# Optimization experiments

Hardware: AMD Instinct MI355X
Metric: run time of the kernel (lower is better)

Reference implementation:

```python
import jax, jax.numpy as jnp
import numpy as np

N_NODES = 80000
N_EDGES = 1280000
IN_C, HID_C, OUT_C = 3, 64, 3
BN_EPS = 1e-5
LEAKY_SLOPE = 0.01  # torch LeakyReLU default
SELF_LOOP_W = 2.0   # GCNConv(improved=True) fill value


def gcn_conv(x, src, dst, n, W, b):
    # PyG GCNConv: x = x @ W, then degree-normalized aggregation with
    # self-loops of weight 2 (improved=True), then + bias.
    h = x @ W  # [N, out]
    deg = jnp.zeros((n,), x.dtype).at[dst].add(1.0) + SELF_LOOP_W  # in-degree + self loop weight
    dinv = jax.lax.rsqrt(deg)
    norm = dinv[src] * dinv[dst]  # per-edge norm (edge_weight = 1)
    agg = jax.ops.segment_sum(h[src] * norm[:, None], dst, num_segments=n)
    self_term = (SELF_LOOP_W * dinv * dinv)[:, None] * h  # self-loop contribution
    return agg + self_term + b


def batch_norm(x, gamma, beta):
    # training-mode BN over the node dimension, biased variance, eps=1e-5
    mean = jnp.mean(x, axis=0)
    var = jnp.mean((x - mean) ** 2, axis=0)
    return (x - mean) * jax.lax.rsqrt(var + BN_EPS) * gamma + beta


def maxpool1d(x, k, p):
    # torch MaxPool1d on a 2D [N, C] tensor pools along C (same-size: stride 1)
    return jax.lax.reduce_window(x, -jnp.inf, jax.lax.max,
                                 (1, k), (1, 1), ((0, 0), (p, p)))


def leaky_relu(x):
    return jnp.where(x >= 0, x, LEAKY_SLOPE * x)


def stage(x, src, dst, n, W, b, gamma, beta, lw, lb, pool_k, pool_p):
    h = gcn_conv(x, src, dst, n, W, b)
    h = batch_norm(h, gamma, beta)
    h = leaky_relu(maxpool1d(h, pool_k, pool_p))
    h = leaky_relu(h @ lw.T + lb)
    return h  # Dropout: eval-mode identity


def setup_inputs() -> dict:
    key = jax.random.key(0)
    ks = jax.random.split(key, 24)
    x = jax.random.normal(ks[0], (N_NODES, IN_C), dtype=jnp.float32)
    edge_index = jax.random.randint(ks[1], (2, N_EDGES), 0, N_NODES, dtype=jnp.int64)

    def lin_init(k, fan_in, shape):
        bound = 1.0 / np.sqrt(fan_in)
        return jax.random.uniform(k, shape, jnp.float32, -bound, bound)

    dims = [(IN_C, HID_C), (HID_C, HID_C), (HID_C, OUT_C)]
    params = {}
    i = 2
    for s, (cin, cout) in enumerate(dims):
        params[f"w{s}"] = lin_init(ks[i], cin, (cin, cout)); i += 1
        params[f"b{s}"] = jnp.zeros((cout,), jnp.float32)
        params[f"g{s}"] = jnp.ones((cout,), jnp.float32)
        params[f"bb{s}"] = jnp.zeros((cout,), jnp.float32)
        params[f"lw{s}"] = lin_init(ks[i], cout, (cout, cout)); i += 1
        params[f"lb{s}"] = lin_init(ks[i], cout, (cout,)); i += 1
    return {"x": x, "edge_index": edge_index, **params}


def reference(x, edge_index, w0, b0, g0, bb0, lw0, lb0,
              w1, b1, g1, bb1, lw1, lb1,
              w2, b2, g2, bb2, lw2, lb2):
    src, dst = edge_index[0], edge_index[1]
    n = x.shape[0]
    h = stage(x, src, dst, n, w0, b0, g0, bb0, lw0, lb0, 3, 1)
    h = stage(h, src, dst, n, w1, b1, g1, bb1, lw1, lb1, 5, 2)
    h = stage(h, src, dst, n, w2, b2, g2, bb2, lw2, lb2, 3, 1)
    return h
```

## Files before the change

kernel.cpp:

```cpp
#include <hip/hip_runtime.h>
#include <hip/hip_bf16.h>
#include <math.h>

#define N_NODES 80000
#define N_EDGES 1280000
#define CHUNK 128
#define N_CHUNKS (N_EDGES / CHUNK)
#define NCB 64
#define CB_DIV 1250
#define CB_CAP 21000
#define NFB 1250
#define FB_CAP 1280
#define EPB 1280
#define ATS 20

typedef __hip_bfloat16 bf16;

__device__ __forceinline__ float leaky(float x) { return x >= 0.f ? x : 0.01f * x; }

union U4 { uint4 v; bf16 h[8]; };


__global__ void k_init(float* bnsums, float* bnrep, int* ctails, int* ftails,
                       const float* __restrict__ lw0, const float* __restrict__ w1,
                       const float* __restrict__ lw1, uint4* __restrict__ pkw) {
    int i = blockIdx.x * 256 + threadIdx.x;
    if (i < 384) bnsums[i] = 0.f;
    if (i < 2048) bnrep[i] = 0.f;
    if (i < NCB) ctails[i] = 0;
    if (i < NFB) ftails[i] = 0;
    if (i >= 1536) return;
    int set = i >> 9, r = i & 511;
    int k = r >> 3, cg = r & 7;
    U4 u;
    if (set == 0) {
#pragma unroll
        for (int j = 0; j < 8; ++j) u.h[j] = __float2bfloat16(lw0[(cg * 8 + j) * 64 + k]);
    } else if (set == 1) {
#pragma unroll
        for (int j = 0; j < 8; ++j) u.h[j] = __float2bfloat16(w1[k * 64 + cg * 8 + j]);
    } else {
#pragma unroll
        for (int j = 0; j < 8; ++j) u.h[j] = __float2bfloat16(lw1[(cg * 8 + j) * 64 + k]);
    }
    pkw[i] = u.v;
}

__global__ void __launch_bounds__(256)
k_part(const int* __restrict__ ei, unsigned int* __restrict__ cpairs,
       int* __restrict__ ctails) {
    __shared__ int cnt[NCB], off[NCB];
    int t = threadIdx.x;
    if (t < NCB) cnt[t] = 0;
    __syncthreads();
    int base = blockIdx.x * EPB;
    unsigned int loc[5];
    int blk[5];
#pragma unroll
    for (int u = 0; u < 5; ++u) {
        int e = base + u * 256 + t;
        int s = ei[e], d = ei[N_EDGES + e];
        int b = d / CB_DIV;
        blk[u] = b;
        loc[u] = (unsigned int)s | ((unsigned int)(d - b * CB_DIV) << 17);
        atomicAdd(&cnt[b], 1);
    }
    __syncthreads();
    if (t < NCB) off[t] = atomicAdd(&ctails[t], cnt[t]);
    __syncthreads();
#pragma unroll
    for (int u = 0; u < 5; ++u) {
        int b = blk[u];
        int pos = atomicAdd(&off[b], 1);
        cpairs[(size_t)b * CB_CAP + pos] = loc[u];
    }
}

__global__ void __launch_bounds__(256)
k_refine(const unsigned int* __restrict__ cpairs, const int* __restrict__ ctails,
         int* __restrict__ ftails, unsigned int* __restrict__ fpairs) {
    __shared__ unsigned int s_ed[2048];
    __shared__ unsigned int s_comp[2048];
    __shared__ int cnt2[32], off2[32], lcl[32], lpos[32];
    int b = blockIdx.x & 63;
    int j = blockIdx.x >> 6;
    int t = threadIdx.x;
    int cnt = ctails[b];
    int s0 = j * 2048;
    if (s0 >= cnt) return;
    int n = min(2048, cnt - s0);
    int fb0 = (b * CB_DIV) >> 6;
    int nbins = (((b + 1) * CB_DIV - 1) >> 6) - fb0 + 1;
    int dbase = b * CB_DIV;
    const unsigned int* lst = cpairs + (size_t)b * CB_CAP + s0;
    for (int i = t; i < n; i += 256) s_ed[i] = lst[i];
    if (t < 32) cnt2[t] = 0;
    __syncthreads();
    for (int i = t; i < n; i += 256) {
        int d = dbase + (int)(s_ed[i] >> 17);
        atomicAdd(&cnt2[(d >> 6) - fb0], 1);
    }
    __syncthreads();
    if (t == 0) {
        int s = 0;
        for (int q = 0; q < nbins; ++q) { lcl[q] = s; s += cnt2[q]; }
    }
    if (t < nbins && cnt2[t] > 0) off2[t] = atomicAdd(&ftails[fb0 + t], cnt2[t]);
    __syncthreads();
    if (t < nbins) lpos[t] = lcl[t];
    __syncthreads();
    for (int i = t; i < n; i += 256) {
        unsigned int r = s_ed[i];
        int d = dbase + (int)(r >> 17);
        int fbl = (d >> 6) - fb0;
        int p = atomicAdd(&lpos[fbl], 1);
        s_comp[p] = (r & 0x1FFFFu) | ((unsigned int)(d & 63) << 20);
    }
    __syncthreads();
    int wv = t >> 6, ln = t & 63;
    for (int q = wv; q < nbins; q += 4) {
        int c = cnt2[q];
        if (c == 0) continue;
        unsigned int* dst = fpairs + (size_t)(fb0 + q) * FB_CAP + off2[q];
        const unsigned int* src = s_comp + lcl[q];
        for (int i = ln; i < c; i += 64) dst[i] = src[i];
    }
}

__global__ void k_scanF(const int* __restrict__ ftails, int* __restrict__ fbase) {
    __shared__ int csum[256];
    int t = threadIdx.x;
    int loc[5];
    int sum = 0;
#pragma unroll
    for (int u = 0; u < 5; ++u) {
        int idx = t * 5 + u;
        int v = (idx < NFB) ? ftails[idx] : 0;
        loc[u] = sum;
        sum += v;
    }
    csum[t] = sum;
    __syncthreads();
    for (int off = 1; off < 256; off <<= 1) {
        int x = (t >= off) ? csum[t - off] : 0;
        __syncthreads();
        csum[t] += x;
        __syncthreads();
    }
    int base = (t > 0) ? csum[t - 1] : 0;
#pragma unroll
    for (int u = 0; u < 5; ++u) {
        int idx = t * 5 + u;
        if (idx < NFB) fbase[idx] = base + loc[u];
    }
}

__global__ void __launch_bounds__(256)
k_sortfine(const unsigned int* __restrict__ fpairs, const int* __restrict__ ftails,
           const int* __restrict__ fbase, int2* __restrict__ ed2,
           float* __restrict__ dinv, int* __restrict__ cursor) {
    __shared__ unsigned int stage[FB_CAP];
    __shared__ int hist[64], cur[64];
    int fb = blockIdx.x;
    int t = threadIdx.x;
    int cnt = ftails[fb];
    int base = fbase[fb];
    int node0 = fb * 64;
    const unsigned int* lst = fpairs + (size_t)fb * FB_CAP;
    if (t < 64) hist[t] = 0;
    __syncthreads();
    for (int i = t; i < cnt; i += 256)
        atomicAdd(&hist[lst[i] >> 20], 1);
    __syncthreads();
    if (t == 0) {
        int s = 0;
        for (int j = 0; j < 64; ++j) { cur[j] = s; s += hist[j]; }
    }
    __syncthreads();
    if (t < 64) {
        cursor[node0 + t] = base + cur[t];
        dinv[node0 + t] = rsqrtf((float)hist[t] + 2.0f);
    }
    __syncthreads();
    for (int i = t; i < cnt; i += 256) {
        unsigned int r = lst[i];
        int p = atomicAdd(&cur[r >> 20], 1);
        stage[p] = r;
    }
    __syncthreads();
    for (int i = t; i < cnt; i += 256) {
        unsigned int r = stage[i];
        ed2[base + i] = make_int2((int)(r & 0xFFFFFu), node0 + (int)(r >> 20));
    }
}

__global__ void k_h0(const float* __restrict__ x, const float* __restrict__ W0,
                     const float* __restrict__ dinv, bf16* __restrict__ hs) {
    int tid = blockIdx.x * blockDim.x + threadIdx.x;
    if (tid < N_NODES * 64) {
        int v = tid >> 6, c = tid & 63;
        float x0 = x[v * 3], x1 = x[v * 3 + 1], x2 = x[v * 3 + 2];
        float h = x0 * W0[c] + x1 * W0[64 + c] + x2 * W0[128 + c];
        hs[tid] = __float2bfloat16(dinv[v] * h);
    }
}


__global__ void __launch_bounds__(256)
k_aggf(const bf16* __restrict__ hs, const int2* __restrict__ ed2,
       const float* __restrict__ dinv, const float* __restrict__ bias,
       float* __restrict__ y, float* __restrict__ bnrep) {
    int lane = threadIdx.x & 63;
    int wid = (blockIdx.x * blockDim.x + threadIdx.x) >> 6;
    float bc = bias[lane];
    float bs = 0.f, bss = 0.f;
    if (wid < N_CHUNKS) {
        int e = wid * CHUNK;
        int dp = (e == 0) ? -1 : ed2[e - 1].y;
        int cur = dp;
        float acc = 0.f;
        float selfv = 0.f, dvc = 0.f;
        int2 c[8];
#pragma unroll
        for (int u = 0; u < 8; ++u) c[u] = ed2[e + u];
        for (int b = 0; b < CHUNK / 8; ++b) {
            float pv[8];
#pragma unroll
            for (int u = 0; u < 8; ++u)
                pv[u] = __bfloat162float(hs[(size_t)c[u].x * 64 + lane]);
            int2 cn[8];
            if (b < CHUNK / 8 - 1) {
#pragma unroll
                for (int u = 0; u < 8; ++u) cn[u] = ed2[e + 8 + u];
            }
#pragma unroll
            for (int u = 0; u < 8; ++u) {
                int du = __builtin_amdgcn_readfirstlane(c[u].y);
                if (du != cur) {
                    if (cur != dp) {
                        float yf = fmaf(dvc, acc + 2.f * selfv, bc);
                        y[(size_t)cur * 64 + lane] = yf;
                        bs += yf; bss += yf * yf;
                    }
                    for (int g = cur + 1; g < du; ++g) {
                        float yf = fmaf(dinv[g],
                                        2.f * __bfloat162float(hs[(size_t)g * 64 + lane]), bc);
                        y[(size_t)g * 64 + lane] = yf;
                        bs += yf; bss += yf * yf;
                    }
                    cur = du;
                    acc = 0.f;
                    selfv = __bfloat162float(hs[(size_t)du * 64 + lane]);
                    dvc = dinv[du];
                }
                acc += pv[u];
            }
            e += 8;
            if (b < CHUNK / 8 - 1) {
#pragma unroll
                for (int u = 0; u < 8; ++u) c[u] = cn[u];
            }
        }
        while (e < N_EDGES) {
            int2 ct[8];
            float pt[8];
#pragma unroll
            for (int u = 0; u < 8; ++u) ct[u] = ed2[min(e + u, N_EDGES - 1)];
#pragma unroll
            for (int u = 0; u < 8; ++u)
                pt[u] = __bfloat162float(hs[(size_t)ct[u].x * 64 + lane]);
            bool contin = true;
#pragma unroll
            for (int u = 0; u < 8; ++u) {
                if (contin && e + u < N_EDGES &&
                    __builtin_amdgcn_readfirstlane(ct[u].y) == cur)
                    acc += pt[u];
                else
                    contin = false;
            }
            e += 8;
            if (!contin) break;
        }
        if (cur != dp) {
            float yf = fmaf(dvc, acc + 2.f * selfv, bc);
            y[(size_t)cur * 64 + lane] = yf;
            bs += yf; bss += yf * yf;
        }
        if (wid == N_CHUNKS - 1) {
            for (int g = cur + 1; g < N_NODES; ++g) {
                float yf = fmaf(dinv[g],
                                2.f * __bfloat162float(hs[(size_t)g * 64 + lane]), bc);
                y[(size_t)g * 64 + lane] = yf;
                bs += yf; bss += yf * yf;
            }
        }
    }
    __shared__ float s1[256], s2[256];
    s1[threadIdx.x] = bs;
    s2[threadIdx.x] = bss;
    __syncthreads();
    if (threadIdx.x < 64) {
        float t1 = s1[threadIdx.x] + s1[threadIdx.x + 64] + s1[threadIdx.x + 128] + s1[threadIdx.x + 192];
        float t2 = s2[threadIdx.x] + s2[threadIdx.x + 64] + s2[threadIdx.x + 128] + s2[threadIdx.x + 192];
        float* dst = bnrep + (blockIdx.x & 7) * 128;
        atomicAdd(&dst[threadIdx.x], t1);
        atomicAdd(&dst[64 + threadIdx.x], t2);
    }
}

template <int P, int MODE>
__global__ void __launch_bounds__(256)
k_post64(const float* __restrict__ y, const float* __restrict__ dinv,
         const float* __restrict__ bnrep,
         const float* __restrict__ g, const float* __restrict__ bb,
         const uint4* __restrict__ lwpk, const float* __restrict__ lb,
         const uint4* __restrict__ Wnpk, const float* __restrict__ Wnf,
         bf16* __restrict__ hsout, float4* __restrict__ hs3) {
    __shared__ float s_aT[4][64 * ATS];
    __shared__ uint4 s_lwT4[64 * 8];
    __shared__ uint4 s_Wn4[MODE == 0 ? 64 * 8 : 1];
    __shared__ float s_Wnf[MODE == 1 ? 64 * 3 : 1];
    int t = threadIdx.x;
    int w = t >> 6, lane = t & 63;
    for (int i = t; i < 512; i += 256) s_lwT4[i] = lwpk[i];
    if constexpr (MODE == 0) {
        for (int i = t; i < 512; i += 256) s_Wn4[i] = Wnpk[i];
    } else {
        for (int i = t; i < 64 * 3; i += 256) s_Wnf[i] = Wnf[i];
    }
    float msum = 0.f, vsum = 0.f;
#pragma unroll
    for (int r = 0; r < 8; ++r) {
        msum += bnrep[r * 128 + lane];
        vsum += bnrep[r * 128 + 64 + lane];
    }
    float inv_n = 1.0f / (float)N_NODES;
    float mean = msum * inv_n;
    float var = fmaxf(vsum * inv_n - mean * mean, 0.f);
    float sc = g[lane] * rsqrtf(var + 1e-5f);
    float sh = bb[lane] - mean * sc;
    int c0 = (lane >> 3) * 8, n0 = (lane & 7) * 2;
    int cg0 = lane >> 3;
    float lbv[8];
#pragma unroll
    for (int i = 0; i < 8; ++i) lbv[i] = lb[c0 + i];
    float* aT = s_aT[w];

    for (int tile = blockIdx.x; tile < N_NODES / 64; tile += gridDim.x) {
        int nbase = tile * 64 + w * 16;
        __syncthreads();
#pragma unroll 4
        for (int i = 0; i < 16; ++i) {
            size_t idx = (size_t)(nbase + i) * 64 + lane;
            float z = fmaf(sc, y[idx], sh);
            float m = z;
#pragma unroll
            for (int d = 1; d <= P; ++d) {
                float up = __shfl(z, lane + d);
                float dn = __shfl(z, lane - d);
                m = fmaxf(m, (lane + d < 64) ? up : -INFINITY);
                m = fmaxf(m, (lane - d >= 0) ? dn : -INFINITY);
            }
            aT[lane * ATS + i] = leaky(m);
        }
        __syncthreads();
        float acc[2][8];
#pragma unroll
        for (int nn = 0; nn < 2; ++nn)
#pragma unroll
            for (int i = 0; i < 8; ++i) acc[nn][i] = lbv[i];
#pragma unroll 8
        for (int k = 0; k < 64; ++k) {
            float2 av = *(const float2*)&aT[k * ATS + n0];
            U4 u; u.v = s_lwT4[k * 8 + cg0];
            float a2[2] = {av.x, av.y};
            float wv[8];
#pragma unroll
            for (int i = 0; i < 8; ++i) wv[i] = __bfloat162float(u.h[i]);
#pragma unroll
            for (int nn = 0; nn < 2; ++nn)
#pragma unroll
                for (int i = 0; i < 8; ++i) acc[nn][i] = fmaf(a2[nn], wv[i], acc[nn][i]);
        }
#pragma unroll
        for (int nn = 0; nn < 2; ++nn)
#pragma unroll
            for (int i = 0; i < 8; ++i) acc[nn][i] = leaky(acc[nn][i]);

#pragma unroll
        for (int i = 0; i < 8; ++i) {
            float2 ov = make_float2(acc[0][i], acc[1][i]);
            *(float2*)&aT[(c0 + i) * ATS + n0] = ov;
        }
        if constexpr (MODE == 0) {
            float acc2[2][8];
#pragma unroll
            for (int nn = 0; nn < 2; ++nn)
#pragma unroll
                for (int i = 0; i < 8; ++i) acc2[nn][i] = 0.f;
#pragma unroll 8
            for (int k = 0; k < 64; ++k) {
                float2 av = *(const float2*)&aT[k * ATS + n0];
                U4 u; u.v = s_Wn4[k * 8 + cg0];
                float a2[2] = {av.x, av.y};
                float wv[8];
#pragma unroll
                for (int i = 0; i < 8; ++i) wv[i] = __bfloat162float(u.h[i]);
#pragma unroll
                for (int nn = 0; nn < 2; ++nn)
#pragma unroll
                    for (int i = 0; i < 8; ++i) acc2[nn][i] = fmaf(a2[nn], wv[i], acc2[nn][i]);
            }
#pragma unroll
            for (int nn = 0; nn < 2; ++nn) {
                int node = nbase + n0 + nn;
                float dv = dinv[node];
                bf16 pk[8];
#pragma unroll
                for (int i = 0; i < 8; ++i) pk[i] = __float2bfloat16(dv * acc2[nn][i]);
                *(uint4*)&hsout[(size_t)node * 64 + c0] = *(uint4*)pk;
            }
        } else {
            float acc3[2][3];
#pragma unroll
            for (int nn = 0; nn < 2; ++nn)
#pragma unroll
                for (int j = 0; j < 3; ++j) acc3[nn][j] = 0.f;
#pragma unroll 8
            for (int k = 0; k < 64; ++k) {
                float2 av = *(const float2*)&aT[k * ATS + n0];
                float a2[2] = {av.x, av.y};
                float w0 = s_Wnf[k * 3 + 0], w1 = s_Wnf[k * 3 + 1], w2v = s_Wnf[k * 3 + 2];
#pragma unroll
                for (int nn = 0; nn < 2; ++nn) {
                    acc3[nn][0] = fmaf(a2[nn], w0, acc3[nn][0]);
                    acc3[nn][1] = fmaf(a2[nn], w1, acc3[nn][1]);
                    acc3[nn][2] = fmaf(a2[nn], w2v, acc3[nn][2]);
                }
            }
            if (c0 == 0) {
#pragma unroll
                for (int nn = 0; nn < 2; ++nn) {
                    int node = nbase + n0 + nn;
                    float dv = dinv[node];
                    hs3[node] = make_float4(dv * acc3[nn][0], dv * acc3[nn][1],
                                            dv * acc3[nn][2], 0.f);
                }
            }
        }
    }
}

__global__ void __launch_bounds__(256)
k_agg3(const float4* __restrict__ hs3, const int* __restrict__ cursor,
       const int2* __restrict__ ed2, const float* __restrict__ dinv,
       const float* __restrict__ b2, float4* __restrict__ y3,
       float* __restrict__ bnsum) {
    int v = blockIdx.x * blockDim.x + threadIdx.x;
    float y0 = 0.f, y1 = 0.f, y2 = 0.f;
    bool valid = v < N_NODES;
    if (valid) {
        int start = cursor[v];
        int end = (v + 1 < N_NODES) ? cursor[v + 1] : N_EDGES;
        float a0 = 0.f, a1 = 0.f, a2 = 0.f;
        int e = start;
        for (; e + 4 <= end; e += 4) {
            int2 c[4];
#pragma unroll
            for (int u = 0; u < 4; ++u) c[u] = ed2[e + u];
#pragma unroll
            for (int u = 0; u < 4; ++u) {
                float4 h = hs3[c[u].x];
                a0 += h.x; a1 += h.y; a2 += h.z;
            }
        }
        for (; e < end; ++e) {
            float4 h = hs3[ed2[e].x];
            a0 += h.x; a1 += h.y; a2 += h.z;
        }
        float dv = dinv[v];
        float4 hsv = hs3[v];
        y0 = dv * (a0 + 2.f * hsv.x) + b2[0];
        y1 = dv * (a1 + 2.f * hsv.y) + b2[1];
        y2 = dv * (a2 + 2.f * hsv.z) + b2[2];
        y3[v] = make_float4(y0, y1, y2, 0.f);
    }
    __shared__ float sm[256];
    float vals[6] = {y0, y1, y2, y0 * y0, y1 * y1, y2 * y2};
    for (int c = 0; c < 6; ++c) {
        sm[threadIdx.x] = valid ? vals[c] : 0.f;
        __syncthreads();
        for (int off = 128; off > 0; off >>= 1) {
            if (threadIdx.x < off) sm[threadIdx.x] += sm[threadIdx.x + off];
            __syncthreads();
        }
        if (threadIdx.x == 0) atomicAdd(&bnsum[c], sm[0]);
        __syncthreads();
    }
}

__global__ void k_post3(const float4* __restrict__ y3, const float* __restrict__ bnsum,
                        const float* __restrict__ g, const float* __restrict__ bb,
                        const float* __restrict__ lw, const float* __restrict__ lb,
                        float* __restrict__ out) {
    int v = blockIdx.x * blockDim.x + threadIdx.x;
    if (v >= N_NODES) return;
    float inv_n = 1.0f / (float)N_NODES;
    float sc[3], sh[3];
#pragma unroll
    for (int c = 0; c < 3; ++c) {
        float mean = bnsum[c] * inv_n;
        float var = fmaxf(bnsum[3 + c] * inv_n - mean * mean, 0.f);
        sc[c] = g[c] * rsqrtf(var + 1e-5f);
        sh[c] = bb[c] - mean * sc[c];
    }
    float4 y = y3[v];
    float z0 = fmaf(y.x, sc[0], sh[0]);
    float z1 = fmaf(y.y, sc[1], sh[1]);
    float z2 = fmaf(y.z, sc[2], sh[2]);
    float p0 = fmaxf(z0, z1);
    float p1 = fmaxf(p0, z2);
    float p2 = fmaxf(z1, z2);
    float a0 = leaky(p0), a1 = leaky(p1), a2 = leaky(p2);
    float o0 = leaky(lb[0] + a0 * lw[0] + a1 * lw[1] + a2 * lw[2]);
    float o1 = leaky(lb[1] + a0 * lw[3] + a1 * lw[4] + a2 * lw[5]);
    float o2 = leaky(lb[2] + a0 * lw[6] + a1 * lw[7] + a2 * lw[8]);
    out[v * 3 + 0] = o0;
    out[v * 3 + 1] = o1;
    out[v * 3 + 2] = o2;
}


extern "C" void kernel_launch(void* const* d_in, const int* in_sizes, int n_in,
                              void* d_out, int out_size, void* d_ws, size_t ws_size,
                              hipStream_t stream) {
    const float* x  = (const float*)d_in[0];
    const int*   ei = (const int*)d_in[1];
    const float* w0 = (const float*)d_in[2];
    const float* b0 = (const float*)d_in[3];
    const float* g0 = (const float*)d_in[4];
    const float* bb0 = (const float*)d_in[5];
    const float* lw0 = (const float*)d_in[6];
    const float* lb0 = (const float*)d_in[7];
    const float* w1 = (const float*)d_in[8];
    const float* b1 = (const float*)d_in[9];
    const float* g1 = (const float*)d_in[10];
    const float* bb1 = (const float*)d_in[11];
    const float* lw1 = (const float*)d_in[12];
    const float* lb1 = (const float*)d_in[13];
    const float* w2 = (const float*)d_in[14];
    const float* b2 = (const float*)d_in[15];
    const float* g2 = (const float*)d_in[16];
    const float* bb2 = (const float*)d_in[17];
    const float* lw2 = (const float*)d_in[18];
    const float* lb2 = (const float*)d_in[19];
    float* out = (float*)d_out;

    char* w = (char*)d_ws;
    float* yagg = (float*)w;       w += (size_t)N_NODES * 64 * 4;
    int2* ed2 = (int2*)w;          w += (size_t)N_EDGES * 8;
    unsigned int* fpairs = (unsigned int*)w; w += (size_t)NFB * FB_CAP * 4;
    bf16* hs = (bf16*)w;           w += (size_t)N_NODES * 64 * 2;
    float4* hs3 = (float4*)w;      w += (size_t)N_NODES * 16;
    float4* y3 = (float4*)w;       w += (size_t)N_NODES * 16;
    int* fbase = (int*)w;          w += (size_t)N_NODES * 4;
    float* dinv = (float*)w;       w += (size_t)N_NODES * 4;
    int* cursor = (int*)w;         w += (size_t)N_NODES * 4;
    int* partial = (int*)w;        w += 512 * 4;
    float* bnsum = (float*)w;      w += 384 * 4;
    int* ctails = (int*)w;         w += NCB * 4;
    int* ftails = (int*)w;         w += NFB * 4;
    (void)partial;
    unsigned int* cpairs = (unsigned int*)yagg;
    uint4* pkw = (uint4*)y3;
    float* bnrep = (float*)((char*)fbase + 16384);

    const int NB = (N_NODES + 255) / 256;

    k_init<<<8, 256, 0, stream>>>(bnsum, bnrep, ctails, ftails, lw0, w1, lw1, pkw);
    k_part<<<N_EDGES / EPB, 256, 0, stream>>>(ei, cpairs, ctails);
    k_refine<<<64 * 16, 256, 0, stream>>>(cpairs, ctails, ftails, fpairs);
    k_scanF<<<1, 256, 0, stream>>>(ftails, fbase);
    k_sortfine<<<NFB, 256, 0, stream>>>(fpairs, ftails, fbase, ed2, dinv, cursor);

    k_h0<<<(N_NODES * 64 + 255) / 256, 256, 0, stream>>>(x, w0, dinv, hs);
    k_aggf<<<2500, 256, 0, stream>>>(hs, ed2, dinv, b0, yagg, bnrep);
    k_post64<1, 0><<<1250, 256, 0, stream>>>(yagg, dinv, bnrep, g0, bb0,
                                             pkw, lb0, pkw + 512, nullptr,
                                             hs, nullptr);

    k_aggf<<<2500, 256, 0, stream>>>(hs, ed2, dinv, b1, yagg, bnrep + 1024);
    k_post64<2, 1><<<1250, 256, 0, stream>>>(yagg, dinv, bnrep + 1024, g1, bb1,
                                             pkw + 1024, lb1, nullptr, w2,
                                             nullptr, hs3);

    k_agg3<<<NB, 256, 0, stream>>>(hs3, cursor, ed2, dinv, b2, y3, bnsum + 256);
    k_post3<<<NB, 256, 0, stream>>>(y3, bnsum + 256, g2, bb2, lw2, lb2, out);
}
```

Baseline: 334.0 us.

## Stage edge records in LDS and double-buffer gathers in CSR aggregation kernel

The aggregation kernel now loads each block's 512 edge records into shared memory with one coalesced int4 load per thread, then has each wave read them from LDS. The inner loop is software-pipelined with two register buffers, so the next group's gathers are issued while the current eight are processed. A fast path sums all eight gathered values when the whole group shares the current destination. The tail continuation only gathers the rows it actually uses. This trades extra LDS use and register pressure for more memory-level parallelism and less edge-index traffic.

```diff
diff --git a/kernel.cpp b/kernel.cpp
--- a/kernel.cpp
+++ b/kernel.cpp
@@ -206,82 +206,113 @@
 }
 
 
+#define PROC8(R, G)                                                              \
+    do {                                                                         \
+        int d7_ = __builtin_amdgcn_readfirstlane(R[7].y);                        \
+        if (d7_ == cur) {                                                        \
+            acc += ((G[0] + G[1]) + (G[2] + G[3])) + ((G[4] + G[5]) + (G[6] + G[7])); \
+        } else {                                                                 \
+            _Pragma("unroll")                                                    \
+            for (int u_ = 0; u_ < 8; ++u_) {                                     \
+                int du_ = __builtin_amdgcn_readfirstlane(R[u_].y);               \
+                if (du_ != cur) {                                                \
+                    if (cur != dp) {                                             \
+                        float yf_ = fmaf(dvc, acc + 2.f * selfv, bc);            \
+                        y[(size_t)cur * 64 + lane] = yf_;                        \
+                        bs += yf_; bss += yf_ * yf_;                             \
+                    }                                                            \
+                    for (int g_ = cur + 1; g_ < du_; ++g_) {                     \
+                        float yf_ = fmaf(dinv[g_],                               \
+                            2.f * __bfloat162float(hs[(size_t)g_ * 64 + lane]), bc); \
+                        y[(size_t)g_ * 64 + lane] = yf_;                         \
+                        bs += yf_; bss += yf_ * yf_;                             \
+                    }                                                            \
+                    cur = du_;                                                   \
+                    acc = 0.f;                                                   \
+                    selfv = __bfloat162float(hs[(size_t)du_ * 64 + lane]);       \
+                    dvc = dinv[du_];                                             \
+                }                                                                \
+                acc += G[u_];                                                    \
+            }                                                                    \
+        }                                                                        \
+    } while (0)
+
 __global__ void __launch_bounds__(256)
 k_aggf(const bf16* __restrict__ hs, const int2* __restrict__ ed2,
        const float* __restrict__ dinv, const float* __restrict__ bias,
        float* __restrict__ y, float* __restrict__ bnrep) {
-    int lane = threadIdx.x & 63;
-    int wid = (blockIdx.x * blockDim.x + threadIdx.x) >> 6;
+    __shared__ int2 s_rec[512];
+    int t = threadIdx.x;
+    int lane = t & 63;
+    int w = t >> 6;
+    ((int4*)s_rec)[t] = ((const int4*)ed2)[(size_t)blockIdx.x * 256 + t];
+    __syncthreads();
+
     float bc = bias[lane];
     float bs = 0.f, bss = 0.f;
-    if (wid < N_CHUNKS) {
-        int e = wid * CHUNK;
-        int dp = (e == 0) ? -1 : ed2[e - 1].y;
+    int wid = blockIdx.x * 4 + w;
+    {
+        int e0 = wid * CHUNK;
+        int rbase = w * CHUNK;
+        int dp = (w > 0) ? s_rec[rbase - 1].y
+                         : ((e0 == 0) ? -1 : ed2[e0 - 1].y);
         int cur = dp;
         float acc = 0.f;
         float selfv = 0.f, dvc = 0.f;
-        int2 c[8];
-#pragma unroll
-        for (int u = 0; u < 8; ++u) c[u] = ed2[e + u];
-        for (int b = 0; b < CHUNK / 8; ++b) {
-            float pv[8];
+
+        int2 rA[8], rB[8];
+        float gA[8], gB[8];
+#pragma unroll
+        for (int u = 0; u < 8; ++u) rA[u] = s_rec[rbase + u];
+#pragma unroll
+        for (int u = 0; u < 8; ++u)
+            gA[u] = __bfloat162float(hs[(size_t)rA[u].x * 64 + lane]);
+#pragma unroll
+        for (int u = 0; u < 8; ++u) rB[u] = s_rec[rbase + 8 + u];
+
+        for (int bb = 0; bb < CHUNK / 16; ++bb) {
 #pragma unroll
             for (int u = 0; u < 8; ++u)
-                pv[u] = __bfloat162float(hs[(size_t)c[u].x * 64 + lane]);
-            int2 cn[8];
-            if (b < CHUNK / 8 - 1) {
-#pragma unroll
-                for (int u = 0; u < 8; ++u) cn[u] = ed2[e + 8 + u];
-            }
-#pragma unroll
-            for (int u = 0; u < 8; ++u) {
-                int du = __builtin_amdgcn_readfirstlane(c[u].y);
-                if (du != cur) {
-                    if (cur != dp) {
-                        float yf = fmaf(dvc, acc + 2.f * selfv, bc);
-                        y[(size_t)cur * 64 + lane] = yf;
-                        bs += yf; bss += yf * yf;
-                    }
-                    for (int g = cur + 1; g < du; ++g) {
-                        float yf = fmaf(dinv[g],
-                                        2.f * __bfloat162float(hs[(size_t)g * 64 + lane]), bc);
-                        y[(size_t)g * 64 + lane] = yf;
-                        bs += yf; bss += yf * yf;
-                    }
-                    cur = du;
-                    acc = 0.f;
-                    selfv = __bfloat162float(hs[(size_t)du * 64 + lane]);
-                    dvc = dinv[du];
+                gB[u] = __bfloat162float(hs[(size_t)rB[u].x * 64 + lane]);
+            PROC8(rA, gA);
+            if (bb < CHUNK / 16 - 1) {
+#pragma unroll
+                for (int u = 0; u < 8; ++u) rA[u] = s_rec[rbase + (2 * bb + 2) * 8 + u];
+#pragma unroll
+                for (int u = 0; u < 8; ++u)
+                    gA[u] = __bfloat162float(hs[(size_t)rA[u].x * 64 + lane]);
+            }
+            PROC8(rB, gB);
+            if (bb < CHUNK / 16 - 1) {
+#pragma unroll
+                for (int u = 0; u < 8; ++u) rB[u] = s_rec[rbase + (2 * bb + 3) * 8 + u];
+            }
+        }
+
+        if (cur != dp) {
+            int e = e0 + CHUNK;
+            while (e < N_EDGES) {
+                int2 ct[8];
+#pragma unroll
+                for (int u = 0; u < 8; ++u) ct[u] = ed2[min(e + u, N_EDGES - 1)];
+                int nb = 0;
+                bool ok = true;
+#pragma unroll
+                for (int u = 0; u < 8; ++u) {
+                    if (ok && e + u < N_EDGES &&
+                        __builtin_amdgcn_readfirstlane(ct[u].y) == cur)
+                        nb++;
+                    else
+                        ok = false;
                 }
-                acc += pv[u];
-            }
-            e += 8;
-            if (b < CHUNK / 8 - 1) {
-#pragma unroll
-                for (int u = 0; u < 8; ++u) c[u] = cn[u];
-            }
-        }
-        while (e < N_EDGES) {
-            int2 ct[8];
-            float pt[8];
-#pragma unroll
-            for (int u = 0; u < 8; ++u) ct[u] = ed2[min(e + u, N_EDGES - 1)];
-#pragma unroll
-            for (int u = 0; u < 8; ++u)
-                pt[u] = __bfloat162float(hs[(size_t)ct[u].x * 64 + lane]);
-            bool contin = true;
-#pragma unroll
-            for (int u = 0; u < 8; ++u) {
-                if (contin && e + u < N_EDGES &&
-                    __builtin_amdgcn_readfirstlane(ct[u].y) == cur)
-                    acc += pt[u];
-                else
-                    contin = false;
-            }
-            e += 8;
-            if (!contin) break;
-        }
-        if (cur != dp) {
+#pragma unroll
+                for (int u = 0; u < 8; ++u) {
+                    if (u < nb)
+                        acc += __bfloat162float(hs[(size_t)ct[u].x * 64 + lane]);
+                }
+                e += 8;
+                if (nb < 8) break;
+            }
             float yf = fmaf(dvc, acc + 2.f * selfv, bc);
             y[(size_t)cur * 64 + lane] = yf;
             bs += yf; bss += yf * yf;
@@ -296,15 +327,15 @@
         }
     }
     __shared__ float s1[256], s2[256];
-    s1[threadIdx.x] = bs;
-    s2[threadIdx.x] = bss;
-    __syncthreads();
-    if (threadIdx.x < 64) {
-        float t1 = s1[threadIdx.x] + s1[threadIdx.x + 64] + s1[threadIdx.x + 128] + s1[threadIdx.x + 192];
-        float t2 = s2[threadIdx.x] + s2[threadIdx.x + 64] + s2[threadIdx.x + 128] + s2[threadIdx.x + 192];
+    s1[t] = bs;
+    s2[t] = bss;
+    __syncthreads();
+    if (t < 64) {
+        float t1 = s1[t] + s1[t + 64] + s1[t + 128] + s1[t + 192];
+        float t2 = s2[t] + s2[t + 64] + s2[t + 128] + s2[t + 192];
         float* dst = bnrep + (blockIdx.x & 7) * 128;
-        atomicAdd(&dst[threadIdx.x], t1);
-        atomicAdd(&dst[64 + threadIdx.x], t2);
+        atomicAdd(&dst[t], t1);
+        atomicAdd(&dst[64 + t], t2);
     }
 }
 
```

After: 331.9 us. No clear change (-0.6%).

## Switch aggregation to CSR source-only edges and fold h0 into sort

Applied to the files above, without the earlier changes.

Edges are stored as source indices only (int instead of int2), and the 64-wide aggregation moves from fixed-size edge chunks with destination-change detection to a per-node CSR loop in which each wavefront handles 8 consecutive nodes using cursor offsets. The layer-0 feature transform is computed inside the fine sort kernel from shared-memory copies of x and W0, which removes a separate launch. This halves index traffic and drops the branchy segment-boundary logic, but load balance now depends on per-node degree rather than equal edge counts.

```diff
diff --git a/kernel.cpp b/kernel.cpp
--- a/kernel.cpp
+++ b/kernel.cpp
@@ -4,8 +4,6 @@
 
 #define N_NODES 80000
 #define N_EDGES 1280000
-#define CHUNK 128
-#define N_CHUNKS (N_EDGES / CHUNK)
 #define NCB 64
 #define CB_DIV 1250
 #define CB_CAP 21000
@@ -157,10 +155,13 @@
 
 __global__ void __launch_bounds__(256)
 k_sortfine(const unsigned int* __restrict__ fpairs, const int* __restrict__ ftails,
-           const int* __restrict__ fbase, int2* __restrict__ ed2,
-           float* __restrict__ dinv, int* __restrict__ cursor) {
+           const int* __restrict__ fbase, int* __restrict__ src4,
+           float* __restrict__ dinv, int* __restrict__ cursor,
+           const float* __restrict__ x, const float* __restrict__ W0,
+           bf16* __restrict__ hs) {
     __shared__ unsigned int stage[FB_CAP];
     __shared__ int hist[64], cur[64];
+    __shared__ float sx[192], sW0[192], sdv[64];
     int fb = blockIdx.x;
     int t = threadIdx.x;
     int cnt = ftails[fb];
@@ -168,9 +169,11 @@
     int node0 = fb * 64;
     const unsigned int* lst = fpairs + (size_t)fb * FB_CAP;
     if (t < 64) hist[t] = 0;
+    if (t >= 64 && t < 256) sW0[t - 64] = W0[t - 64];
     __syncthreads();
     for (int i = t; i < cnt; i += 256)
         atomicAdd(&hist[lst[i] >> 20], 1);
+    for (int i = t; i < 192; i += 256) sx[i] = x[(size_t)node0 * 3 + i];
     __syncthreads();
     if (t == 0) {
         int s = 0;
@@ -179,7 +182,9 @@
     __syncthreads();
     if (t < 64) {
         cursor[node0 + t] = base + cur[t];
-        dinv[node0 + t] = rsqrtf((float)hist[t] + 2.0f);
+        float dv = rsqrtf((float)hist[t] + 2.0f);
+        dinv[node0 + t] = dv;
+        sdv[t] = dv;
     }
     __syncthreads();
     for (int i = t; i < cnt; i += 256) {
@@ -188,123 +193,72 @@
         stage[p] = r;
     }
     __syncthreads();
-    for (int i = t; i < cnt; i += 256) {
-        unsigned int r = stage[i];
-        ed2[base + i] = make_int2((int)(r & 0xFFFFFu), node0 + (int)(r >> 20));
-    }
-}
-
-__global__ void k_h0(const float* __restrict__ x, const float* __restrict__ W0,
-                     const float* __restrict__ dinv, bf16* __restrict__ hs) {
-    int tid = blockIdx.x * blockDim.x + threadIdx.x;
-    if (tid < N_NODES * 64) {
-        int v = tid >> 6, c = tid & 63;
-        float x0 = x[v * 3], x1 = x[v * 3 + 1], x2 = x[v * 3 + 2];
-        float h = x0 * W0[c] + x1 * W0[64 + c] + x2 * W0[128 + c];
-        hs[tid] = __float2bfloat16(dinv[v] * h);
+    for (int i = t; i < cnt; i += 256)
+        src4[base + i] = (int)(stage[i] & 0xFFFFFu);
+    for (int i = t; i < 4096; i += 256) {
+        int v = i >> 6, c = i & 63;
+        float h = sx[v * 3] * sW0[c] + sx[v * 3 + 1] * sW0[64 + c] + sx[v * 3 + 2] * sW0[128 + c];
+        hs[(size_t)(node0 + v) * 64 + c] = __float2bfloat16(sdv[v] * h);
     }
 }
 
 
 __global__ void __launch_bounds__(256)
-k_aggf(const bf16* __restrict__ hs, const int2* __restrict__ ed2,
-       const float* __restrict__ dinv, const float* __restrict__ bias,
-       float* __restrict__ y, float* __restrict__ bnrep) {
-    int lane = threadIdx.x & 63;
-    int wid = (blockIdx.x * blockDim.x + threadIdx.x) >> 6;
+k_aggc(const bf16* __restrict__ hs, const int* __restrict__ src4,
+       const int* __restrict__ cursor, const float* __restrict__ dinv,
+       const float* __restrict__ bias, float* __restrict__ y,
+       float* __restrict__ bnrep) {
+    int t = threadIdx.x, lane = t & 63, w = t >> 6;
+    int v0 = (blockIdx.x * 4 + w) * 8;
     float bc = bias[lane];
     float bs = 0.f, bss = 0.f;
-    if (wid < N_CHUNKS) {
-        int e = wid * CHUNK;
-        int dp = (e == 0) ? -1 : ed2[e - 1].y;
-        int cur = dp;
+    int e = __builtin_amdgcn_readfirstlane(cursor[v0]);
+#pragma unroll 1
+    for (int v = v0; v < v0 + 8; ++v) {
+        int rend = __builtin_amdgcn_readfirstlane(
+            (v + 1 < N_NODES) ? cursor[v + 1] : N_EDGES);
         float acc = 0.f;
-        float selfv = 0.f, dvc = 0.f;
-        int2 c[8];
-#pragma unroll
-        for (int u = 0; u < 8; ++u) c[u] = ed2[e + u];
-        for (int b = 0; b < CHUNK / 8; ++b) {
-            float pv[8];
+        while (e + 16 <= rend) {
+            int sv[16];
+            float gv[16];
+#pragma unroll
+            for (int u = 0; u < 16; ++u) sv[u] = src4[e + u];
+#pragma unroll
+            for (int u = 0; u < 16; ++u)
+                gv[u] = __bfloat162float(hs[(size_t)sv[u] * 64 + lane]);
+            float p1 = ((gv[0] + gv[1]) + (gv[2] + gv[3])) + ((gv[4] + gv[5]) + (gv[6] + gv[7]));
+            float p2 = ((gv[8] + gv[9]) + (gv[10] + gv[11])) + ((gv[12] + gv[13]) + (gv[14] + gv[15]));
+            acc += p1 + p2;
+            e += 16;
+        }
+        if (e + 8 <= rend) {
+            int sv[8];
+            float gv[8];
+#pragma unroll
+            for (int u = 0; u < 8; ++u) sv[u] = src4[e + u];
 #pragma unroll
             for (int u = 0; u < 8; ++u)
-                pv[u] = __bfloat162float(hs[(size_t)c[u].x * 64 + lane]);
-            int2 cn[8];
-            if (b < CHUNK / 8 - 1) {
-#pragma unroll
-                for (int u = 0; u < 8; ++u) cn[u] = ed2[e + 8 + u];
-            }
-#pragma unroll
-            for (int u = 0; u < 8; ++u) {
-                int du = __builtin_amdgcn_readfirstlane(c[u].y);
-                if (du != cur) {
-                    if (cur != dp) {
-                        float yf = fmaf(dvc, acc + 2.f * selfv, bc);
-                        y[(size_t)cur * 64 + lane] = yf;
-                        bs += yf; bss += yf * yf;
-                    }
-                    for (int g = cur + 1; g < du; ++g) {
-                        float yf = fmaf(dinv[g],
-                                        2.f * __bfloat162float(hs[(size_t)g * 64 + lane]), bc);
-                        y[(size_t)g * 64 + lane] = yf;
-                        bs += yf; bss += yf * yf;
-                    }
-                    cur = du;
-                    acc = 0.f;
-                    selfv = __bfloat162float(hs[(size_t)du * 64 + lane]);
-                    dvc = dinv[du];
-                }
-                acc += pv[u];
-            }
+                gv[u] = __bfloat162float(hs[(size_t)sv[u] * 64 + lane]);
+            acc += ((gv[0] + gv[1]) + (gv[2] + gv[3])) + ((gv[4] + gv[5]) + (gv[6] + gv[7]));
             e += 8;
-            if (b < CHUNK / 8 - 1) {
-#pragma unroll
-                for (int u = 0; u < 8; ++u) c[u] = cn[u];
-            }
-        }
-        while (e < N_EDGES) {
-            int2 ct[8];
-            float pt[8];
-#pragma unroll
-            for (int u = 0; u < 8; ++u) ct[u] = ed2[min(e + u, N_EDGES - 1)];
-#pragma unroll
-            for (int u = 0; u < 8; ++u)
-                pt[u] = __bfloat162float(hs[(size_t)ct[u].x * 64 + lane]);
-            bool contin = true;
-#pragma unroll
-            for (int u = 0; u < 8; ++u) {
-                if (contin && e + u < N_EDGES &&
-                    __builtin_amdgcn_readfirstlane(ct[u].y) == cur)
-                    acc += pt[u];
-                else
-                    contin = false;
-            }
-            e += 8;
-            if (!contin) break;
-        }
-        if (cur != dp) {
-            float yf = fmaf(dvc, acc + 2.f * selfv, bc);
-            y[(size_t)cur * 64 + lane] = yf;
-            bs += yf; bss += yf * yf;
-        }
-        if (wid == N_CHUNKS - 1) {
-            for (int g = cur + 1; g < N_NODES; ++g) {
-                float yf = fmaf(dinv[g],
-                                2.f * __bfloat162float(hs[(size_t)g * 64 + lane]), bc);
-                y[(size_t)g * 64 + lane] = yf;
-                bs += yf; bss += yf * yf;
-            }
-        }
+        }
+        for (; e < rend; ++e)
+            acc += __bfloat162float(hs[(size_t)src4[e] * 64 + lane]);
+        float yf = fmaf(dinv[v], acc + 2.f * __bfloat162float(hs[(size_t)v * 64 + lane]), bc);
+        y[(size_t)v * 64 + lane] = yf;
+        bs += yf;
+        bss += yf * yf;
     }
     __shared__ float s1[256], s2[256];
-    s1[threadIdx.x] = bs;
-    s2[threadIdx.x] = bss;
-    __syncthreads();
-    if (threadIdx.x < 64) {
-        float t1 = s1[threadIdx.x] + s1[threadIdx.x + 64] + s1[threadIdx.x + 128] + s1[threadIdx.x + 192];
-        float t2 = s2[threadIdx.x] + s2[threadIdx.x + 64] + s2[threadIdx.x + 128] + s2[threadIdx.x + 192];
+    s1[t] = bs;
+    s2[t] = bss;
+    __syncthreads();
+    if (t < 64) {
+        float t1 = s1[t] + s1[t + 64] + s1[t + 128] + s1[t + 192];
+        float t2 = s2[t] + s2[t + 64] + s2[t + 128] + s2[t + 192];
         float* dst = bnrep + (blockIdx.x & 7) * 128;
-        atomicAdd(&dst[threadIdx.x], t1);
-        atomicAdd(&dst[64 + threadIdx.x], t2);
+        atomicAdd(&dst[t], t1);
+        atomicAdd(&dst[64 + t], t2);
     }
 }
 
@@ -453,7 +407,7 @@
 
 __global__ void __launch_bounds__(256)
 k_agg3(const float4* __restrict__ hs3, const int* __restrict__ cursor,
-       const int2* __restrict__ ed2, const float* __restrict__ dinv,
+       const int* __restrict__ src4, const float* __restrict__ dinv,
        const float* __restrict__ b2, float4* __restrict__ y3,
        float* __restrict__ bnsum) {
     int v = blockIdx.x * blockDim.x + threadIdx.x;
@@ -465,17 +419,17 @@
         float a0 = 0.f, a1 = 0.f, a2 = 0.f;
         int e = start;
         for (; e + 4 <= end; e += 4) {
-            int2 c[4];
-#pragma unroll
-            for (int u = 0; u < 4; ++u) c[u] = ed2[e + u];
+            int c[4];
+#pragma unroll
+            for (int u = 0; u < 4; ++u) c[u] = src4[e + u];
 #pragma unroll
             for (int u = 0; u < 4; ++u) {
-                float4 h = hs3[c[u].x];
+                float4 h = hs3[c[u]];
                 a0 += h.x; a1 += h.y; a2 += h.z;
             }
         }
         for (; e < end; ++e) {
-            float4 h = hs3[ed2[e].x];
+            float4 h = hs3[src4[e]];
             a0 += h.x; a1 += h.y; a2 += h.z;
         }
         float dv = dinv[v];
@@ -558,7 +512,7 @@
 
     char* w = (char*)d_ws;
     float* yagg = (float*)w;       w += (size_t)N_NODES * 64 * 4;
-    int2* ed2 = (int2*)w;          w += (size_t)N_EDGES * 8;
+    int* src4 = (int*)w;           w += (size_t)N_EDGES * 8;
     unsigned int* fpairs = (unsigned int*)w; w += (size_t)NFB * FB_CAP * 4;
     bf16* hs = (bf16*)w;           w += (size_t)N_NODES * 64 * 2;
     float4* hs3 = (float4*)w;      w += (size_t)N_NODES * 16;
@@ -581,19 +535,19 @@
     k_part<<<N_EDGES / EPB, 256, 0, stream>>>(ei, cpairs, ctails);
     k_refine<<<64 * 16, 256, 0, stream>>>(cpairs, ctails, ftails, fpairs);
     k_scanF<<<1, 256, 0, stream>>>(ftails, fbase);
-    k_sortfine<<<NFB, 256, 0, stream>>>(fpairs, ftails, fbase, ed2, dinv, cursor);
-
-    k_h0<<<(N_NODES * 64 + 255) / 256, 256, 0, stream>>>(x, w0, dinv, hs);
-    k_aggf<<<2500, 256, 0, stream>>>(hs, ed2, dinv, b0, yagg, bnrep);
+    k_sortfine<<<NFB, 256, 0, stream>>>(fpairs, ftails, fbase, src4, dinv, cursor,
+                                        x, w0, hs);
+
+    k_aggc<<<2500, 256, 0, stream>>>(hs, src4, cursor, dinv, b0, yagg, bnrep);
     k_post64<1, 0><<<1250, 256, 0, stream>>>(yagg, dinv, bnrep, g0, bb0,
                                              pkw, lb0, pkw + 512, nullptr,
                                              hs, nullptr);
 
-    k_aggf<<<2500, 256, 0, stream>>>(hs, ed2, dinv, b1, yagg, bnrep + 1024);
+    k_aggc<<<2500, 256, 0, stream>>>(hs, src4, cursor, dinv, b1, yagg, bnrep + 1024);
     k_post64<2, 1><<<1250, 256, 0, stream>>>(yagg, dinv, bnrep + 1024, g1, bb1,
                                              pkw + 1024, lb1, nullptr, w2,
                                              nullptr, hs3);
 
-    k_agg3<<<NB, 256, 0, stream>>>(hs3, cursor, ed2, dinv, b2, y3, bnsum + 256);
+    k_agg3<<<NB, 256, 0, stream>>>(hs3, cursor, src4, dinv, b2, y3, bnsum + 256);
     k_post3<<<NB, 256, 0, stream>>>(y3, bnsum + 256, g2, bb2, lw2, lb2, out);
 }
```

Measured after the change: 335.2 us. About the same (+0.4%).
